# Kernel tuning notes

Hardware: AMD Instinct MI355X
Metric: run time of the kernel (lower is better)

## Reference

```python
import jax, jax.numpy as jnp
import numpy as np

EPS = 1e-5

def conv1x1(x, w, b):
    # x: [B,Cin,H,W], w: [Cout,Cin], b: [Cout]
    return jnp.einsum('oi,bihw->bohw', w, x) + b[None, :, None, None]

def self_attention(x, qw, qb, kw, kb, vw, vb, fw, fb):
    B, C, H, W = x.shape
    hid = qw.shape[0]
    q = conv1x1(x, qw, qb).reshape(B, hid, H * W).transpose(0, 2, 1)   # [B,HW,hid]
    k = conv1x1(x, kw, kb).reshape(B, hid, H * W)                      # [B,hid,HW]
    v = conv1x1(x, vw, vb).reshape(B, C, H * W)                        # [B,C,HW]
    attn = jax.nn.softmax(jnp.einsum('bnh,bhm->bnm', q, k), axis=-1)   # [B,HW,HW]
    z = jnp.einsum('bnm,bcm->bnc', attn, v)                            # [B,HW,C]
    # faithful to torch .view(B,C,H,W) on contiguous [B,HW,C]: raw reshape, no transpose
    z = z.reshape(B, C, H, W)
    return conv1x1(z * x, fw, fb) + x

def group_norm_per_channel(y, gw, gb):
    # GroupNorm(num_groups == num_channels): per-channel instance norm, biased var
    mean = y.mean(axis=(2, 3), keepdims=True)
    var = ((y - mean) ** 2).mean(axis=(2, 3), keepdims=True)
    yn = (y - mean) * jax.lax.rsqrt(var + EPS)
    return yn * gw[None, :, None, None] + gb[None, :, None, None]

def setup_inputs() -> dict:
    key = jax.random.key(0)
    ks = jax.random.split(key, 32)
    B, C, H, W = 4, 64, 64, 64
    hid, att = 64, 64
    d = {}
    d['x'] = jax.random.normal(ks[0], (B, C, H, W), jnp.float32)
    d['h'] = jax.random.normal(ks[1], (B, hid, H, W), jnp.float32)
    d['c'] = jax.random.normal(ks[2], (B, hid, H, W), jnp.float32)
    i = 3
    for pre, cin in (('ax', C), ('ah', hid)):
        for nm, cout in (('q', att), ('k', att), ('v', cin), ('f', cin)):
            d[f'{pre}_{nm}w'] = jax.random.normal(ks[i], (cout, cin), jnp.float32) * 0.05; i += 1
            d[f'{pre}_{nm}b'] = jax.random.normal(ks[i], (cout,), jnp.float32) * 0.05; i += 1
    d['conv_w'] = jax.random.normal(ks[i], (4 * hid, C + hid, 3, 3), jnp.float32) * 0.05; i += 1
    d['conv_b'] = jax.random.normal(ks[i], (4 * hid,), jnp.float32) * 0.05; i += 1
    d['gn_w'] = jnp.ones((4 * hid,), jnp.float32)
    d['gn_b'] = jnp.zeros((4 * hid,), jnp.float32)
    return d

def reference(x, h, c,
              ax_qw, ax_qb, ax_kw, ax_kb, ax_vw, ax_vb, ax_fw, ax_fb,
              ah_qw, ah_qb, ah_kw, ah_kb, ah_vw, ah_vb, ah_fw, ah_fb,
              conv_w, conv_b, gn_w, gn_b):
    hid = h.shape[1]
    xa = self_attention(x, ax_qw, ax_qb, ax_kw, ax_kb, ax_vw, ax_vb, ax_fw, ax_fb)
    ha = self_attention(h, ah_qw, ah_qb, ah_kw, ah_kb, ah_vw, ah_vb, ah_fw, ah_fb)
    combined = jnp.concatenate([xa, ha], axis=1)
    y = jax.lax.conv_general_dilated(
        combined, conv_w, window_strides=(1, 1), padding=[(1, 1), (1, 1)],
        dimension_numbers=('NCHW', 'OIHW', 'NCHW')) + conv_b[None, :, None, None]
    y = group_norm_per_channel(y, gn_w, gn_b)
    i, f, o, g = jnp.split(y, 4, axis=1)
    i = jax.nn.sigmoid(i); f = jax.nn.sigmoid(f); o = jax.nn.sigmoid(o); g = jnp.tanh(g)
    c_next = f * c + i * g
    h_next = o * jnp.tanh(c_next)
    return jnp.stack([h_next, c_next])  # [2,B,hid,H,W]
```

## Files before the change

kernel.cpp:

```cpp
#include <hip/hip_runtime.h>
#include <hip/hip_bf16.h>


typedef __hip_bfloat16 bf16;
typedef const __hip_bfloat16* bfp;
typedef short bf16x8 __attribute__((ext_vector_type(8)));
typedef short short4v __attribute__((ext_vector_type(4)));
typedef float f32x4 __attribute__((ext_vector_type(4)));
typedef float f32x16 __attribute__((ext_vector_type(16)));
typedef unsigned int u32x4 __attribute__((ext_vector_type(4)));

#define SM_SHIFT 12.0f
#define SM_A  184.66496523378733f
#define SM_B  14034.452417194552f

__device__ __forceinline__ float ldf(const void* p, long i, int f32) {
    return f32 ? ((const float*)p)[i]
               : __bfloat162float(((const bf16*)p)[i]);
}
__device__ __forceinline__ short f2bf(float f) {
    bf16 h = __float2bfloat16(f);
    return *reinterpret_cast<short*>(&h);
}
__device__ __forceinline__ float bfv(short s) {
    unsigned short u = (unsigned short)s;
    return __bfloat162float(*reinterpret_cast<const bf16*>(&u));
}

__device__ __forceinline__ int sniff_f32(const void* xr)
{
    int lane = threadIdx.x & 63;
    unsigned long long v = ((const unsigned long long*)xr)[lane];
    int ok = 0;
#pragma unroll
    for (int i = 0; i < 4; ++i) {
        int e = (int)((v >> (16 * i + 7)) & 0xFF);
        ok += (e >= 100 && e <= 141);
    }
    ok += __shfl_xor(ok, 1, 64);
    ok += __shfl_xor(ok, 2, 64);
    ok += __shfl_xor(ok, 4, 64);
    ok += __shfl_xor(ok, 8, 64);
    ok += __shfl_xor(ok, 16, 64);
    ok += __shfl_xor(ok, 32, 64);
    return ok < 200;
}

__global__ __launch_bounds__(256) void qkv_kernel(
    const void* __restrict__ Xx, const void* __restrict__ Xh,
    const void* __restrict__ qwx, const void* __restrict__ qbx,
    const void* __restrict__ kwx, const void* __restrict__ kbx,
    const void* __restrict__ vwx, const void* __restrict__ vbx,
    const void* __restrict__ qwh, const void* __restrict__ qbh,
    const void* __restrict__ kwh, const void* __restrict__ kbh,
    const void* __restrict__ vwh, const void* __restrict__ vbh,
    bf16* __restrict__ Qx, bf16* __restrict__ Kx, bf16* __restrict__ Vtx,
    bf16* __restrict__ Qh, bf16* __restrict__ Kh, bf16* __restrict__ Vth,
    const void* __restrict__ cw, bf16* __restrict__ Wt,
    float* __restrict__ gacc, int qkvN)
{
    __shared__ __align__(16) short xt[64][72];
    __shared__ __align__(16) short wq[64][72];
    __shared__ __align__(16) short wk[64][72];
    __shared__ __align__(16) short wv[64][72];
    int bx = blockIdx.x;
    int tid = threadIdx.x;
    int f32 = sniff_f32(Xx);
    if (bx >= qkvN) {
        if (bx == qkvN) {
            for (int j = 0; j < 8; ++j)
                gacc[tid * 8 + j] = 0.f;
        }
        short* tl = &xt[0][0];
        int t = bx - qkvN;
        long sbase = (long)t * 2304;
        if (!f32) {
            const short* cw16 = (const short*)cw;
            for (int j = tid; j < 288; j += 256) {
                bf16x8 v = *(const bf16x8*)(cw16 + sbase + j * 8);
#pragma unroll
                for (int e = 0; e < 8; ++e) {
                    int local = j * 8 + e;
                    int ocl = local / 1152, rem = local % 1152;
                    int ic = rem / 9, tap = rem % 9;
                    tl[ocl * 1152 + tap * 128 + ic] = v[e];
                }
            }
        } else {
            for (int j = tid; j < 2304; j += 256) {
                int ocl = j / 1152, rem = j % 1152;
                int ic = rem / 9, tap = rem % 9;
                tl[ocl * 1152 + tap * 128 + ic] =
                    f2bf(((const float*)cw)[sbase + j]);
            }
        }
        __syncthreads();
        for (int j = tid; j < 288; j += 256) {
            int d = j * 8;
            int ocl = d / 1152, rem = d % 1152;
            int tap = rem / 128, ic0 = rem % 128;
            bf16x8 v = *(const bf16x8*)(tl + ocl * 1152 + tap * 128 + ic0);
            *(bf16x8*)((short*)Wt + (long)tap * 32768
                       + (long)(t * 2 + ocl) * 128 + ic0) = v;
        }
        return;
    }
    int ab  = (bx >> 8) & 1;
    int idx = bx & 255;
    int b = idx >> 6;
    int n0 = (idx & 63) * 64;
    int wave = tid >> 6, lane = tid & 63;
    int q = lane >> 4, l15 = lane & 15;

    const void* X = ab ? Xh : Xx;
    const void* qw = ab ? qwh : qwx; const void* qb = ab ? qbh : qbx;
    const void* kw = ab ? kwh : kwx; const void* kb = ab ? kbh : kbx;
    const void* vw = ab ? vwh : vwx; const void* vb = ab ? vbh : vbx;
    short* Qg  = (short*)(ab ? Qh  : Qx)  + (long)b * 262144;
    short* Kg  = (short*)(ab ? Kh  : Kx)  + (long)b * 262144;
    short* Vtg = (short*)(ab ? Vth : Vtx) + (long)b * 262144;

    if (!f32) {
        const short* q16 = (const short*)qw;
        const short* k16 = (const short*)kw;
        const short* v16 = (const short*)vw;
        for (int rep = 0; rep < 2; ++rep) {
            int j8 = (rep * 256 + tid) * 8;
            *(bf16x8*)&wq[j8 >> 6][j8 & 63] = *(const bf16x8*)(q16 + j8);
            *(bf16x8*)&wk[j8 >> 6][j8 & 63] = *(const bf16x8*)(k16 + j8);
            *(bf16x8*)&wv[j8 >> 6][j8 & 63] = *(const bf16x8*)(v16 + j8);
        }
    } else {
        for (int rep = 0; rep < 16; ++rep) {
            int j = rep * 256 + tid;
            int i = j >> 6, cc = j & 63;
            wq[i][cc] = f2bf(((const float*)qw)[j]);
            wk[i][cc] = f2bf(((const float*)kw)[j]);
            wv[i][cc] = f2bf(((const float*)vw)[j]);
        }
    }
    long xbase = (long)b * 262144;
    if (!f32) {
        const short* X16 = (const short*)X;
        for (int rep = 0; rep < 2; ++rep) {
            int c = rep * 32 + (tid >> 3);
            int p8 = (tid & 7) * 8;
            bf16x8 v = *(const bf16x8*)(X16 + xbase + (long)c * 4096 + n0 + p8);
#pragma unroll
            for (int j = 0; j < 8; ++j) xt[p8 + j][c] = v[j];
        }
    } else {
        for (int rep = 0; rep < 16; ++rep) {
            int c = rep * 4 + (tid >> 6);
            int p = tid & 63;
            xt[p][c] = f2bf(ldf(X, xbase + (long)c * 4096 + n0 + p, f32));
        }
    }
    __syncthreads();

    bf16x8 a0 = *(const bf16x8*)&xt[wave * 16 + l15][q * 8];
    bf16x8 a1 = *(const bf16x8*)&xt[wave * 16 + l15][32 + q * 8];

    float qreg[4][4], kreg[4][4];
    for (int ct = 0; ct < 4; ++ct) {
        bf16x8 bq0 = *(const bf16x8*)&wq[ct * 16 + l15][q * 8];
        bf16x8 bq1 = *(const bf16x8*)&wq[ct * 16 + l15][32 + q * 8];
        f32x4 z = (f32x4){0.f, 0.f, 0.f, 0.f};
        z = __builtin_amdgcn_mfma_f32_16x16x32_bf16(a0, bq0, z, 0, 0, 0);
        z = __builtin_amdgcn_mfma_f32_16x16x32_bf16(a1, bq1, z, 0, 0, 0);
        float bias = ldf(qb, ct * 16 + l15, f32);
        for (int reg = 0; reg < 4; ++reg) qreg[ct][reg] = z[reg] + bias;
    }
    for (int ct = 0; ct < 4; ++ct) {
        bf16x8 bk0 = *(const bf16x8*)&wk[ct * 16 + l15][q * 8];
        bf16x8 bk1 = *(const bf16x8*)&wk[ct * 16 + l15][32 + q * 8];
        f32x4 z = (f32x4){0.f, 0.f, 0.f, 0.f};
        z = __builtin_amdgcn_mfma_f32_16x16x32_bf16(a0, bk0, z, 0, 0, 0);
        z = __builtin_amdgcn_mfma_f32_16x16x32_bf16(a1, bk1, z, 0, 0, 0);
        float bias = ldf(kb, ct * 16 + l15, f32);
        for (int reg = 0; reg < 4; ++reg) kreg[ct][reg] = z[reg] + bias;
    }
    __syncthreads();
#pragma unroll
    for (int ct = 0; ct < 4; ++ct)
#pragma unroll
        for (int reg = 0; reg < 4; ++reg) {
            wq[wave * 16 + q * 4 + reg][ct * 16 + l15] = f2bf(qreg[ct][reg]);
            wk[wave * 16 + q * 4 + reg][ct * 16 + l15] = f2bf(kreg[ct][reg]);
        }
    __syncthreads();
    {
        int r = tid >> 2;
        int c0 = (tid & 3) * 16;
        *(bf16x8*)(Qg + (long)(n0 + r) * 64 + c0)     = *(const bf16x8*)&wq[r][c0];
        *(bf16x8*)(Qg + (long)(n0 + r) * 64 + c0 + 8) = *(const bf16x8*)&wq[r][c0 + 8];
        *(bf16x8*)(Kg + (long)(n0 + r) * 64 + c0)     = *(const bf16x8*)&wk[r][c0];
        *(bf16x8*)(Kg + (long)(n0 + r) * 64 + c0 + 8) = *(const bf16x8*)&wk[r][c0 + 8];
    }
    bf16x8 av0 = *(const bf16x8*)&wv[wave * 16 + l15][q * 8];
    bf16x8 av1 = *(const bf16x8*)&wv[wave * 16 + l15][32 + q * 8];
    for (int ct = 0; ct < 4; ++ct) {
        bf16x8 bx0 = *(const bf16x8*)&xt[ct * 16 + l15][q * 8];
        bf16x8 bx1 = *(const bf16x8*)&xt[ct * 16 + l15][32 + q * 8];
        f32x4 z = (f32x4){0.f, 0.f, 0.f, 0.f};
        z = __builtin_amdgcn_mfma_f32_16x16x32_bf16(av0, bx0, z, 0, 0, 0);
        z = __builtin_amdgcn_mfma_f32_16x16x32_bf16(av1, bx1, z, 0, 0, 0);
        for (int reg = 0; reg < 4; ++reg) {
            int c_out = wave * 16 + q * 4 + reg;
            float bias = ldf(vb, c_out, f32);
            Vtg[(long)c_out * 4096 + n0 + ct * 16 + l15] = f2bf(z[reg] + bias);
        }
    }
}

__global__ __launch_bounds__(512, 4) void attn_kernel(
    bfp Qx, bfp Kx, bfp Vtx,
    const void* __restrict__ Xx, const void* __restrict__ fwx,
    const void* __restrict__ fbx, bf16* __restrict__ outx,
    bfp Qh, bfp Kh, bfp Vth,
    const void* __restrict__ Xh, const void* __restrict__ fwh,
    const void* __restrict__ fbh, bf16* __restrict__ outh)
{
    __shared__ __align__(16) short smem[32768];

    int tid = threadIdx.x;
    int wave = tid >> 6, lane = tid & 63;
    int l31 = lane & 31, hi = lane >> 5;
    int nh = wave >> 2, mq = wave & 3;
    int bid = blockIdx.x;
    int ab, b, hrow;
    if (gridDim.x == 512) {
        int abb = bid & 7;
        ab = abb >> 2; b = abb & 3;
        hrow = bid >> 3;
    } else {
        ab = 0; b = bid & 3;
        hrow = bid >> 2;
    }
    int f32 = sniff_f32(Xx);

    const short* Qb  = (const short*)(ab ? Qh  : Qx)  + (long)b * 262144;
    const short* Kb  = (const short*)(ab ? Kh  : Kx)  + (long)b * 262144;
    const short* Vtb = (const short*)(ab ? Vth : Vtx) + (long)b * 262144;
    const void* X  = ab ? Xh  : Xx;
    const void* fw = ab ? fwh : fwx;
    const void* fb = ab ? fbh : fbx;
    bf16* out = ab ? outh : outx;
    long xbase = (long)b * 262144;

    int cnq = nh * 32 + l31;
    long nq = (long)cnq * 64 + hrow;
    bf16x8 aq[4];
#pragma unroll
    for (int kc = 0; kc < 4; ++kc)
        aq[kc] = *(const bf16x8*)(Qb + nq * 64 + kc * 16 + hi * 8);

    f32x16 acc[2];
    acc[0] = (f32x16)(0.0f); acc[1] = (f32x16)(0.0f);
    f32x16 acc_l = (f32x16)(0.0f);
    const short ONE = 0x3F80;
    const bf16x8 ones = {ONE, ONE, ONE, ONE, ONE, ONE, ONE, ONE};

    int krow = mq * 32 + l31;
    int swk = ((krow >> 1) ^ (krow >> 4)) & 7;
    int cR0 = l31, cR1 = 32 + l31;
    int kv0 = (cR0 ^ (cR0 >> 3)) & 7;
    int kv1 = (cR1 ^ (cR1 >> 3)) & 7;

    int r0 = tid >> 3, r1 = r0 + 64;
    int g = tid & 7;
    int sr0 = (r0 & 51) | ((r0 & 4) << 1) | ((r0 & 8) >> 1);
    int sr1 = sr0 + 64;
    int gk0 = (g ^ (((sr0 >> 1) ^ (sr0 >> 4)) & 7)) << 3;
    int gk1 = (g ^ (((sr1 >> 1) ^ (sr1 >> 4)) & 7)) << 3;
    int cV = r0;
    int gv = (g ^ ((cV ^ (cV >> 3)) & 7)) << 3;

    bf16x8 pk0 = *(const bf16x8*)(Kb + (long)r0 * 64 + g * 8);
    bf16x8 pk1 = *(const bf16x8*)(Kb + (long)r1 * 64 + g * 8);
    bf16x8 pv0 = *(const bf16x8*)(Vtb + (long)cV * 4096 + g * 8);
    bf16x8 pv1 = *(const bf16x8*)(Vtb + (long)cV * 4096 + 64 + g * 8);

    for (int mt = 0; mt < 32; ++mt) {
        int buf = mt & 1;
        short* ksw = smem + buf * 8192;
        short* vsw = smem + 16384 + buf * 8192;
        *(bf16x8*)(ksw + sr0 * 64 + gk0)     = pk0;
        *(bf16x8*)(ksw + sr1 * 64 + gk1)     = pk1;
        *(bf16x8*)(vsw + cV * 128 + gv)      = pv0;
        *(bf16x8*)(vsw + cV * 128 + gv + 64) = pv1;
        __syncthreads();
        if (mt + 1 < 32) {
            long m = (long)(mt + 1) * 128;
            pk0 = *(const bf16x8*)(Kb + (m + r0) * 64 + g * 8);
            pk1 = *(const bf16x8*)(Kb + (m + r1) * 64 + g * 8);
            pv0 = *(const bf16x8*)(Vtb + (long)cV * 4096 + m + g * 8);
            pv1 = *(const bf16x8*)(Vtb + (long)cV * 4096 + m + 64 + g * 8);
        }
        const short* ksb  = smem + buf * 8192;
        const short* vtsb = smem + 16384 + buf * 8192;

        f32x16 s = (f32x16)(0.0f);
        const short* kbase = ksb + krow * 64;
#pragma unroll
        for (int kc = 0; kc < 4; ++kc) {
            bf16x8 ak = *(const bf16x8*)(kbase + (((kc * 2 + hi) ^ swk) << 3));
            s = __builtin_amdgcn_mfma_f32_32x32x16_bf16(ak, aq[kc], s, 0, 0, 0);
        }

        unsigned P32[8];
#pragma unroll
        for (int i = 0; i < 8; ++i) {
            unsigned b0 = (unsigned)fmaxf(fmaf(s[2 * i],     SM_A, SM_B), 0.f);
            unsigned b1 = (unsigned)fmaxf(fmaf(s[2 * i + 1], SM_A, SM_B), 0.f);
            P32[i] = b0 | (b1 << 16);
        }
        u32x4 B0v = (u32x4){P32[0], P32[1], P32[2], P32[3]};
        u32x4 B1v = (u32x4){P32[4], P32[5], P32[6], P32[7]};
        bf16x8 bp0 = __builtin_bit_cast(bf16x8, B0v);
        bf16x8 bp1 = __builtin_bit_cast(bf16x8, B1v);

        acc_l = __builtin_amdgcn_mfma_f32_32x32x16_bf16(ones, bp0, acc_l, 0, 0, 0);
        acc_l = __builtin_amdgcn_mfma_f32_32x32x16_bf16(ones, bp1, acc_l, 0, 0, 0);

#pragma unroll
        for (int mc = 0; mc < 2; ++mc) {
            bf16x8 bp = mc ? bp1 : bp0;
            int qch = mq * 4 + mc * 2 + hi;
            bf16x8 av0 = *(const bf16x8*)(
                vtsb + cR0 * 128 + ((qch ^ kv0) << 3));
            bf16x8 av1 = *(const bf16x8*)(
                vtsb + cR1 * 128 + ((qch ^ kv1) << 3));
            acc[0] = __builtin_amdgcn_mfma_f32_32x32x16_bf16(av0, bp, acc[0], 0, 0, 0);
            acc[1] = __builtin_amdgcn_mfma_f32_32x32x16_bf16(av1, bp, acc[1], 0, 0, 0);
        }
    }

    float l_acc = acc_l[0];

    float* fs = (float*)smem;
    float* fl = (float*)smem + 8192;
    short* fwt_s = smem + 16896;
    short* o_lds = smem + 21504;
    short* at_s  = smem;

    __syncthreads();
    if (hi == 0) fl[nh * 128 + mq * 32 + l31] = l_acc;
    if (mq == 1 || mq == 3) {
        int L = mq >> 1;
#pragma unroll
        for (int ch = 0; ch < 2; ++ch)
#pragma unroll
            for (int r = 0; r < 16; ++r) {
                int c = ch * 32 + (r & 3) + ((r >> 2) << 3) + (hi << 2);
                fs[L * 4096 + nh * 2048 + c * 32 + l31] = acc[ch][r];
            }
    }
    if (!f32) {
        int j8 = tid * 8;
        *(bf16x8*)(fwt_s + (j8 >> 6) * 72 + (j8 & 63)) =
            *(const bf16x8*)((const short*)fw + j8);
    } else {
#pragma unroll
        for (int jj = 0; jj < 8; ++jj) {
            int j = tid * 8 + jj;
            fwt_s[(j >> 6) * 72 + (j & 63)] = f2bf(((const float*)fw)[j]);
        }
    }
    __syncthreads();
    if (mq == 0 || mq == 2) {
        int L = mq >> 1;
#pragma unroll
        for (int ch = 0; ch < 2; ++ch)
#pragma unroll
            for (int r = 0; r < 16; ++r) {
                int c = ch * 32 + (r & 3) + ((r >> 2) << 3) + (hi << 2);
                acc[ch][r] += fs[L * 4096 + nh * 2048 + c * 32 + l31];
            }
    }
    __syncthreads();
    if (mq == 2) {
#pragma unroll
        for (int ch = 0; ch < 2; ++ch)
#pragma unroll
            for (int r = 0; r < 16; ++r) {
                int c = ch * 32 + (r & 3) + ((r >> 2) << 3) + (hi << 2);
                fs[nh * 2048 + c * 32 + l31] = acc[ch][r];
            }
    }
    __syncthreads();
    if (mq == 0) {
        float l_tot = fl[nh * 128 + l31]      + fl[nh * 128 + 32 + l31]
                    + fl[nh * 128 + 64 + l31] + fl[nh * 128 + 96 + l31];
        float iln = 1.f / l_tot;
        short* orow = o_lds + cnq * 68;
#pragma unroll
        for (int ch = 0; ch < 2; ++ch)
#pragma unroll
            for (int rq = 0; rq < 4; ++rq) {
                short4v o4;
#pragma unroll
                for (int j = 0; j < 4; ++j) {
                    int r = rq * 4 + j;
                    int c = ch * 32 + (r & 3) + ((r >> 2) << 3) + (hi << 2);
                    o4[j] = f2bf((acc[ch][r] +
                                  fs[nh * 2048 + c * 32 + l31]) * iln);
                }
                *(short4v*)(orow + ch * 32 + rq * 8 + hi * 4) = o4;
            }
    }
    __syncthreads();
    {
        int cn = tid >> 3;
        int w8 = (tid & 7) * 8;
        if (!f32) {
            bf16x8 xv = *(const bf16x8*)(
                (const short*)X + xbase + (long)cn * 4096 + hrow * 64 + w8);
#pragma unroll
            for (int j = 0; j < 8; ++j)
                at_s[(w8 + j) * 78 + cn] =
                    f2bf(bfv(o_lds[cn * 68 + w8 + j]) * bfv(xv[j]));
        } else {
#pragma unroll
            for (int j = 0; j < 8; ++j)
                at_s[(w8 + j) * 78 + cn] =
                    f2bf(bfv(o_lds[cn * 68 + w8 + j]) *
                         ((const float*)X)[xbase + (long)cn * 4096 + hrow * 64 + w8 + j]);
        }
    }
    __syncthreads();
    {
        int q = lane >> 4, l15 = lane & 15;
        int w4 = wave & 3;
        int ntb = (wave >> 2) * 2;
        bf16x8 a0 = *(const bf16x8*)(fwt_s + (w4 * 16 + l15) * 72 + q * 8);
        bf16x8 a1 = *(const bf16x8*)(fwt_s + (w4 * 16 + l15) * 72 + 32 + q * 8);
        short* outp = (short*)out;
        for (int nt = ntb; nt < ntb + 2; ++nt) {
            bf16x8 b0 = *(const bf16x8*)(at_s + (nt * 16 + l15) * 78 + q * 8);
            bf16x8 b1 = *(const bf16x8*)(at_s + (nt * 16 + l15) * 78 + 32 + q * 8);
            f32x4 z = (f32x4){0.f, 0.f, 0.f, 0.f};
            z = __builtin_amdgcn_mfma_f32_16x16x32_bf16(a0, b0, z, 0, 0, 0);
            z = __builtin_amdgcn_mfma_f32_16x16x32_bf16(a1, b1, z, 0, 0, 0);
            int w = nt * 16 + l15;
            short4v o4;
            for (int reg = 0; reg < 4; ++reg) {
                int o = w4 * 16 + q * 4 + reg;
                float v = z[reg] + ldf(fb, o, f32) +
                          ldf(X, xbase + (long)o * 4096 + hrow * 64 + w, f32);
                o4[reg] = f2bf(v);
            }
            *(short4v*)(outp + (((long)(b * 64 + hrow) * 64 + w) * 64
                                + w4 * 16 + q * 4)) = o4;
        }
    }
}

__global__ __launch_bounds__(512) void conv3x3_kernel(
    bfp xa, bfp ha, bfp Wt, const void* __restrict__ cb,
    bf16* __restrict__ y, float* __restrict__ gacc,
    const void* __restrict__ xraw)
{
    __shared__ __align__(16) short in_s[3][66][136];
    int f32 = sniff_f32(xraw);
    int bx = blockIdx.x;
    int b = bx >> 6;
    int h = bx & 63;
    int tid = threadIdx.x;
    int wave = tid >> 6, lane = tid & 63;
    int q = lane >> 4, l15 = lane & 15;

    const short* xab = (const short*)xa + (long)b * 262144;
    const short* hab = (const short*)ha + (long)b * 262144;
    const bf16x8 zv = {0, 0, 0, 0, 0, 0, 0, 0};
    for (int r = 0; r < 3; ++r) {
        int gy = h + r - 1;
        bool valid = (gy >= 0) && (gy < 64);
        int w = tid >> 3;
        int c8 = (tid & 7) * 8;
        bf16x8 vx = zv, vh = zv;
        if (valid) {
            vx = *(const bf16x8*)(xab + ((long)gy * 64 + w) * 64 + c8);
            vh = *(const bf16x8*)(hab + ((long)gy * 64 + w) * 64 + c8);
        }
        *(bf16x8*)&in_s[r][w + 1][c8]      = vx;
        *(bf16x8*)&in_s[r][w + 1][64 + c8] = vh;
    }
    if (tid < 96) {
        int r = tid / 32;
        int rest = tid % 32;
        int col = (rest & 1) ? 65 : 0;
        int c8 = (rest >> 1) * 8;
        *(bf16x8*)&in_s[r][col][c8] = zv;
    }
    __syncthreads();

    int oc0 = wave * 32;
    f32x4 acc[2][4];
    for (int mt = 0; mt < 2; ++mt)
        for (int nt = 0; nt < 4; ++nt)
            acc[mt][nt] = (f32x4){0.f, 0.f, 0.f, 0.f};

    const short* Wb = (const short*)Wt;
    for (int tap = 0; tap < 9; ++tap) {
        int dy = tap / 3, dx = tap - dy * 3;
        for (int kc = 0; kc < 4; ++kc) {
            bf16x8 afrag[2];
            for (int mt = 0; mt < 2; ++mt)
                afrag[mt] = *(const bf16x8*)(
                    Wb + ((long)tap * 256 + oc0 + mt * 16 + l15) * 128 + kc * 32 + q * 8);
            for (int nt = 0; nt < 4; ++nt) {
                bf16x8 bfrag = *(const bf16x8*)&in_s[dy][nt * 16 + l15 + dx][kc * 32 + q * 8];
                for (int mt = 0; mt < 2; ++mt)
                    acc[mt][nt] = __builtin_amdgcn_mfma_f32_16x16x32_bf16(
                        afrag[mt], bfrag, acc[mt][nt], 0, 0, 0);
            }
        }
    }

    long ybase = (long)b * 1048576 + (long)h * 64;
    for (int mt = 0; mt < 2; ++mt) {
        for (int reg = 0; reg < 4; ++reg) {
            int oc = oc0 + mt * 16 + q * 4 + reg;
            float bias = ldf(cb, oc, f32);
            float s = 0.f, s2 = 0.f;
            for (int nt = 0; nt < 4; ++nt) {
                float v = acc[mt][nt][reg] + bias;
                ((short*)y)[ybase + (long)oc * 4096 + nt * 16 + l15] = f2bf(v);
                s += v; s2 = fmaf(v, v, s2);
            }
            s  += __shfl_xor(s,  1, 64);  s2 += __shfl_xor(s2, 1, 64);
            s  += __shfl_xor(s,  2, 64);  s2 += __shfl_xor(s2, 2, 64);
            s  += __shfl_xor(s,  4, 64);  s2 += __shfl_xor(s2, 4, 64);
            s  += __shfl_xor(s,  8, 64);  s2 += __shfl_xor(s2, 8, 64);
            if (l15 == 0) {
                atomicAdd(&gacc[b * 256 + oc], s);
                atomicAdd(&gacc[1024 + b * 256 + oc], s2);
            }
        }
    }
}

__global__ __launch_bounds__(256) void gates_kernel(
    bfp y, const float* __restrict__ gacc,
    const void* __restrict__ gw, const void* __restrict__ gb,
    const void* __restrict__ c_in, void* __restrict__ out)
{
    int f32 = sniff_f32(c_in);
    int t = blockIdx.x * 256 + threadIdx.x;
    int b = t >> 15;
    int r = t & 32767;
    int ch = r >> 9;
    int p8 = (r & 511) * 8;
    long ybase = (long)b * 1048576;
    long idx8 = (long)b * 262144 + (long)ch * 4096 + p8;

    float mu[4], rstd[4], gwv[4], gbv[4];
    bf16x8 yv[4];
#pragma unroll
    for (int g = 0; g < 4; ++g) {
        int cc = g * 64 + ch;
        float m = gacc[b * 256 + cc] * (1.f / 4096.f);
        float var = gacc[1024 + b * 256 + cc] * (1.f / 4096.f) - m * m;
        mu[g] = m;
        rstd[g] = rsqrtf(fmaxf(var, 0.f) + 1e-5f);
        gwv[g] = ldf(gw, cc, f32);
        gbv[g] = ldf(gb, cc, f32);
        yv[g] = *(const bf16x8*)((const short*)y + ybase + (long)cc * 4096 + p8);
    }
    float cprev[8];
    if (!f32) {
        bf16x8 cv = *(const bf16x8*)((const short*)c_in + idx8);
#pragma unroll
        for (int j = 0; j < 8; ++j) cprev[j] = bfv(cv[j]);
    } else {
#pragma unroll
        for (int j = 0; j < 8; ++j) cprev[j] = ((const float*)c_in)[idx8 + j];
    }
    bf16x8 hn8, cn8;
    float hnf[8], cnf[8];
#pragma unroll
    for (int j = 0; j < 8; ++j) {
        float v0 = (bfv(yv[0][j]) - mu[0]) * rstd[0] * gwv[0] + gbv[0];
        float v1 = (bfv(yv[1][j]) - mu[1]) * rstd[1] * gwv[1] + gbv[1];
        float v2 = (bfv(yv[2][j]) - mu[2]) * rstd[2] * gwv[2] + gbv[2];
        float v3 = (bfv(yv[3][j]) - mu[3]) * rstd[3] * gwv[3] + gbv[3];
        float ig = 1.f / (1.f + __expf(-v0));
        float fg = 1.f / (1.f + __expf(-v1));
        float og = 1.f / (1.f + __expf(-v2));
        float gg = tanhf(v3);
        float cn = fg * cprev[j] + ig * gg;
        float hn = og * tanhf(cn);
        hn8[j] = f2bf(hn); cn8[j] = f2bf(cn);
        hnf[j] = hn; cnf[j] = cn;
    }
    if (f32) {
        float* o32 = (float*)out;
#pragma unroll
        for (int j = 0; j < 8; ++j) {
            o32[idx8 + j] = hnf[j];
            o32[1048576 + idx8 + j] = cnf[j];
        }
    } else {
        short* o16 = (short*)out;
        *(bf16x8*)(o16 + idx8) = hn8;
        *(bf16x8*)(o16 + 1048576 + idx8) = cn8;
    }
}

extern "C" void kernel_launch(void* const* d_in, const int* in_sizes, int n_in,
                              void* d_out, int out_size, void* d_ws, size_t ws_size,
                              hipStream_t stream)
{
    const void* x = d_in[0]; const void* h = d_in[1]; const void* c = d_in[2];
    const void* ax_qw = d_in[3],  *ax_qb = d_in[4];
    const void* ax_kw = d_in[5],  *ax_kb = d_in[6];
    const void* ax_vw = d_in[7],  *ax_vb = d_in[8];
    const void* ax_fw = d_in[9],  *ax_fb = d_in[10];
    const void* ah_qw = d_in[11], *ah_qb = d_in[12];
    const void* ah_kw = d_in[13], *ah_kb = d_in[14];
    const void* ah_vw = d_in[15], *ah_vb = d_in[16];
    const void* ah_fw = d_in[17], *ah_fb = d_in[18];
    const void* conv_w = d_in[19], *conv_b = d_in[20];
    const void* gn_w = d_in[21],  *gn_b = d_in[22];

    char* wsb = (char*)d_ws;
    auto S = [&](int i) { return wsb + ((unsigned long)i << 21); };
    bool fused = ws_size >= (18ul << 20) + 16384;

    bf16* ha = (bf16*)S(0);
    bf16* Wt = (bf16*)S(1);
    bf16 *Qx, *Kx, *Vtx, *Qh, *Kh, *Vth, *xa, *y;
    char* tail;
    if (fused) {
        Qx = (bf16*)S(2); Kx = (bf16*)S(3); Vtx = (bf16*)S(4);
        Qh = (bf16*)S(5); Kh = (bf16*)S(6); Vth = (bf16*)S(7);
        xa = (bf16*)S(8); y = Qx;
        tail = S(9);
    } else {
        Qx = (bf16*)S(2); Kx = (bf16*)S(3); Vtx = (bf16*)S(4);
        Qh = Qx; Kh = Kx; Vth = Vtx;
        xa = (bf16*)S(6); y = Qx;
        tail = S(7);
    }
    float* gacc = (float*)tail;

    if (fused) {
        qkv_kernel<<<512 + 128, 256, 0, stream>>>(
            x, h,
            ax_qw, ax_qb, ax_kw, ax_kb, ax_vw, ax_vb,
            ah_qw, ah_qb, ah_kw, ah_kb, ah_vw, ah_vb,
            Qx, Kx, Vtx, Qh, Kh, Vth, conv_w, Wt, gacc, 512);
        attn_kernel<<<512, 512, 0, stream>>>(
            Qx, Kx, Vtx, x, ax_fw, ax_fb, xa,
            Qh, Kh, Vth, h, ah_fw, ah_fb, ha);
    } else {
        qkv_kernel<<<256 + 128, 256, 0, stream>>>(
            x, x,
            ax_qw, ax_qb, ax_kw, ax_kb, ax_vw, ax_vb,
            ax_qw, ax_qb, ax_kw, ax_kb, ax_vw, ax_vb,
            Qx, Kx, Vtx, Qx, Kx, Vtx, conv_w, Wt, gacc, 256);
        attn_kernel<<<256, 512, 0, stream>>>(
            Qx, Kx, Vtx, x, ax_fw, ax_fb, xa,
            Qx, Kx, Vtx, x, ax_fw, ax_fb, xa);
        qkv_kernel<<<256, 256, 0, stream>>>(
            h, h,
            ah_qw, ah_qb, ah_kw, ah_kb, ah_vw, ah_vb,
            ah_qw, ah_qb, ah_kw, ah_kb, ah_vw, ah_vb,
            Qh, Kh, Vth, Qh, Kh, Vth, conv_w, Wt, gacc, 256);
        attn_kernel<<<256, 512, 0, stream>>>(
            Qh, Kh, Vth, h, ah_fw, ah_fb, ha,
            Qh, Kh, Vth, h, ah_fw, ah_fb, ha);
    }
    conv3x3_kernel<<<256, 512, 0, stream>>>(xa, ha, Wt, conv_b, y, gacc, x);
    gates_kernel<<<512, 256, 0, stream>>>(y, gacc, gn_w, gn_b, c, d_out);
}
```

Baseline: 203.0 us.

## Fuse GroupNorm+LSTM gates into conv3x3 via grid-wide barrier, keep y in LDS

The conv3x3 kernel now keeps its output tile in shared memory instead of writing y to global memory. After a grid-wide atomic-counter barrier across all 256 blocks, it reads the finished per-channel statistics and applies GroupNorm and the LSTM gate math directly. This removes the separate gates kernel launch and the global round-trip of y. The barrier relies on all 256 blocks being co-resident and adds spin-wait latency. The counter is reset inside qkv_kernel, at gacc[2048], which matches the tail+8192 offset.

New measurement: 258.9 us. 27.5% more time.

```diff
diff --git a/kernel.cpp b/kernel.cpp
--- a/kernel.cpp
+++ b/kernel.cpp
@@ -70,6 +70,7 @@
         if (bx == qkvN) {
             for (int j = 0; j < 8; ++j)
                 gacc[tid * 8 + j] = 0.f;
+            if (tid == 0) ((unsigned*)gacc)[2048] = 0u;
         }
         short* tl = &xt[0][0];
         int t = bx - qkvN;
@@ -458,10 +459,12 @@
 
 __global__ __launch_bounds__(512) void conv3x3_kernel(
     bfp xa, bfp ha, bfp Wt, const void* __restrict__ cb,
-    bf16* __restrict__ y, float* __restrict__ gacc,
+    float* __restrict__ gacc, unsigned* __restrict__ cnt,
+    const void* __restrict__ gw, const void* __restrict__ gb,
+    const void* __restrict__ c_in, void* __restrict__ out,
     const void* __restrict__ xraw)
 {
-    __shared__ __align__(16) short in_s[3][66][136];
+    __shared__ __align__(16) short cs[26928];
     int f32 = sniff_f32(xraw);
     int bx = blockIdx.x;
     int b = bx >> 6;
@@ -483,15 +486,15 @@
             vx = *(const bf16x8*)(xab + ((long)gy * 64 + w) * 64 + c8);
             vh = *(const bf16x8*)(hab + ((long)gy * 64 + w) * 64 + c8);
         }
-        *(bf16x8*)&in_s[r][w + 1][c8]      = vx;
-        *(bf16x8*)&in_s[r][w + 1][64 + c8] = vh;
+        *(bf16x8*)(cs + r * 8976 + (w + 1) * 136 + c8)      = vx;
+        *(bf16x8*)(cs + r * 8976 + (w + 1) * 136 + 64 + c8) = vh;
     }
     if (tid < 96) {
         int r = tid / 32;
         int rest = tid % 32;
         int col = (rest & 1) ? 65 : 0;
         int c8 = (rest >> 1) * 8;
-        *(bf16x8*)&in_s[r][col][c8] = zv;
+        *(bf16x8*)(cs + r * 8976 + col * 136 + c8) = zv;
     }
     __syncthreads();
 
@@ -510,7 +513,8 @@
                 afrag[mt] = *(const bf16x8*)(
                     Wb + ((long)tap * 256 + oc0 + mt * 16 + l15) * 128 + kc * 32 + q * 8);
             for (int nt = 0; nt < 4; ++nt) {
-                bf16x8 bfrag = *(const bf16x8*)&in_s[dy][nt * 16 + l15 + dx][kc * 32 + q * 8];
+                bf16x8 bfrag = *(const bf16x8*)(
+                    cs + dy * 8976 + (nt * 16 + l15 + dx) * 136 + kc * 32 + q * 8);
                 for (int mt = 0; mt < 2; ++mt)
                     acc[mt][nt] = __builtin_amdgcn_mfma_f32_16x16x32_bf16(
                         afrag[mt], bfrag, acc[mt][nt], 0, 0, 0);
@@ -518,7 +522,8 @@
         }
     }
 
-    long ybase = (long)b * 1048576 + (long)h * 64;
+    __syncthreads();
+    short* y_s = cs;
     for (int mt = 0; mt < 2; ++mt) {
         for (int reg = 0; reg < 4; ++reg) {
             int oc = oc0 + mt * 16 + q * 4 + reg;
@@ -526,7 +531,7 @@
             float s = 0.f, s2 = 0.f;
             for (int nt = 0; nt < 4; ++nt) {
                 float v = acc[mt][nt][reg] + bias;
-                ((short*)y)[ybase + (long)oc * 4096 + nt * 16 + l15] = f2bf(v);
+                y_s[oc * 66 + nt * 16 + l15] = f2bf(v);
                 s += v; s2 = fmaf(v, v, s2);
             }
             s  += __shfl_xor(s,  1, 64);  s2 += __shfl_xor(s2, 1, 64);
@@ -539,72 +544,69 @@
             }
         }
     }
-}
-
-__global__ __launch_bounds__(256) void gates_kernel(
-    bfp y, const float* __restrict__ gacc,
-    const void* __restrict__ gw, const void* __restrict__ gb,
-    const void* __restrict__ c_in, void* __restrict__ out)
-{
-    int f32 = sniff_f32(c_in);
-    int t = blockIdx.x * 256 + threadIdx.x;
-    int b = t >> 15;
-    int r = t & 32767;
-    int ch = r >> 9;
-    int p8 = (r & 511) * 8;
-    long ybase = (long)b * 1048576;
-    long idx8 = (long)b * 262144 + (long)ch * 4096 + p8;
-
-    float mu[4], rstd[4], gwv[4], gbv[4];
-    bf16x8 yv[4];
-#pragma unroll
-    for (int g = 0; g < 4; ++g) {
-        int cc = g * 64 + ch;
-        float m = gacc[b * 256 + cc] * (1.f / 4096.f);
-        float var = gacc[1024 + b * 256 + cc] * (1.f / 4096.f) - m * m;
-        mu[g] = m;
-        rstd[g] = rsqrtf(fmaxf(var, 0.f) + 1e-5f);
-        gwv[g] = ldf(gw, cc, f32);
-        gbv[g] = ldf(gb, cc, f32);
-        yv[g] = *(const bf16x8*)((const short*)y + ybase + (long)cc * 4096 + p8);
-    }
-    float cprev[8];
-    if (!f32) {
-        bf16x8 cv = *(const bf16x8*)((const short*)c_in + idx8);
-#pragma unroll
-        for (int j = 0; j < 8; ++j) cprev[j] = bfv(cv[j]);
-    } else {
-#pragma unroll
-        for (int j = 0; j < 8; ++j) cprev[j] = ((const float*)c_in)[idx8 + j];
-    }
-    bf16x8 hn8, cn8;
-    float hnf[8], cnf[8];
-#pragma unroll
-    for (int j = 0; j < 8; ++j) {
-        float v0 = (bfv(yv[0][j]) - mu[0]) * rstd[0] * gwv[0] + gbv[0];
-        float v1 = (bfv(yv[1][j]) - mu[1]) * rstd[1] * gwv[1] + gbv[1];
-        float v2 = (bfv(yv[2][j]) - mu[2]) * rstd[2] * gwv[2] + gbv[2];
-        float v3 = (bfv(yv[3][j]) - mu[3]) * rstd[3] * gwv[3] + gbv[3];
-        float ig = 1.f / (1.f + __expf(-v0));
-        float fg = 1.f / (1.f + __expf(-v1));
-        float og = 1.f / (1.f + __expf(-v2));
-        float gg = tanhf(v3);
-        float cn = fg * cprev[j] + ig * gg;
-        float hn = og * tanhf(cn);
-        hn8[j] = f2bf(hn); cn8[j] = f2bf(cn);
-        hnf[j] = hn; cnf[j] = cn;
-    }
-    if (f32) {
-        float* o32 = (float*)out;
+    __threadfence();
+    if (tid == 0) {
+        atomicAdd(cnt, 1u);
+        while (atomicAdd(cnt, 0u) < 256u) { __builtin_amdgcn_s_sleep(8); }
+    }
+    __syncthreads();
+    __threadfence();
+
+    {
+        int ch = tid >> 3;
+        int px8 = (tid & 7) * 8;
+        float mu[4], rstd[4], gwv[4], gbv[4];
+        bf16x8 yv[4];
+#pragma unroll
+        for (int g = 0; g < 4; ++g) {
+            int cc = g * 64 + ch;
+            float m = gacc[b * 256 + cc] * (1.f / 4096.f);
+            float var = gacc[1024 + b * 256 + cc] * (1.f / 4096.f) - m * m;
+            mu[g] = m;
+            rstd[g] = rsqrtf(fmaxf(var, 0.f) + 1e-5f);
+            gwv[g] = ldf(gw, cc, f32);
+            gbv[g] = ldf(gb, cc, f32);
+            yv[g] = *(const bf16x8*)(y_s + (g * 64 + ch) * 66 + px8);
+        }
+        long idx8 = (long)b * 262144 + (long)ch * 4096 + h * 64 + px8;
+        float cprev[8];
+        if (!f32) {
+            bf16x8 cv = *(const bf16x8*)((const short*)c_in + idx8);
+#pragma unroll
+            for (int j = 0; j < 8; ++j) cprev[j] = bfv(cv[j]);
+        } else {
+#pragma unroll
+            for (int j = 0; j < 8; ++j) cprev[j] = ((const float*)c_in)[idx8 + j];
+        }
+        bf16x8 hn8, cn8;
+        float hnf[8], cnf[8];
 #pragma unroll
         for (int j = 0; j < 8; ++j) {
-            o32[idx8 + j] = hnf[j];
-            o32[1048576 + idx8 + j] = cnf[j];
-        }
-    } else {
-        short* o16 = (short*)out;
-        *(bf16x8*)(o16 + idx8) = hn8;
-        *(bf16x8*)(o16 + 1048576 + idx8) = cn8;
+            float v0 = (bfv(yv[0][j]) - mu[0]) * rstd[0] * gwv[0] + gbv[0];
+            float v1 = (bfv(yv[1][j]) - mu[1]) * rstd[1] * gwv[1] + gbv[1];
+            float v2 = (bfv(yv[2][j]) - mu[2]) * rstd[2] * gwv[2] + gbv[2];
+            float v3 = (bfv(yv[3][j]) - mu[3]) * rstd[3] * gwv[3] + gbv[3];
+            float ig = 1.f / (1.f + __expf(-v0));
+            float fg = 1.f / (1.f + __expf(-v1));
+            float og = 1.f / (1.f + __expf(-v2));
+            float gg = tanhf(v3);
+            float cn = fg * cprev[j] + ig * gg;
+            float hn = og * tanhf(cn);
+            hn8[j] = f2bf(hn); cn8[j] = f2bf(cn);
+            hnf[j] = hn; cnf[j] = cn;
+        }
+        if (f32) {
+            float* o32 = (float*)out;
+#pragma unroll
+            for (int j = 0; j < 8; ++j) {
+                o32[idx8 + j] = hnf[j];
+                o32[1048576 + idx8 + j] = cnf[j];
+            }
+        } else {
+            short* o16 = (short*)out;
+            *(bf16x8*)(o16 + idx8) = hn8;
+            *(bf16x8*)(o16 + 1048576 + idx8) = cn8;
+        }
     }
 }
 
@@ -630,20 +632,21 @@
 
     bf16* ha = (bf16*)S(0);
     bf16* Wt = (bf16*)S(1);
-    bf16 *Qx, *Kx, *Vtx, *Qh, *Kh, *Vth, *xa, *y;
+    bf16 *Qx, *Kx, *Vtx, *Qh, *Kh, *Vth, *xa;
     char* tail;
     if (fused) {
         Qx = (bf16*)S(2); Kx = (bf16*)S(3); Vtx = (bf16*)S(4);
         Qh = (bf16*)S(5); Kh = (bf16*)S(6); Vth = (bf16*)S(7);
-        xa = (bf16*)S(8); y = Qx;
+        xa = (bf16*)S(8);
         tail = S(9);
     } else {
         Qx = (bf16*)S(2); Kx = (bf16*)S(3); Vtx = (bf16*)S(4);
         Qh = Qx; Kh = Kx; Vth = Vtx;
-        xa = (bf16*)S(6); y = Qx;
+        xa = (bf16*)S(6);
         tail = S(7);
     }
     float* gacc = (float*)tail;
+    unsigned* cnt = (unsigned*)(tail + 8192);
 
     if (fused) {
         qkv_kernel<<<512 + 128, 256, 0, stream>>>(
@@ -672,6 +675,6 @@
             Qh, Kh, Vth, h, ah_fw, ah_fb, ha,
             Qh, Kh, Vth, h, ah_fw, ah_fb, ha);
     }
-    conv3x3_kernel<<<256, 512, 0, stream>>>(xa, ha, Wt, conv_b, y, gacc, x);
-    gates_kernel<<<512, 256, 0, stream>>>(y, gacc, gn_w, gn_b, c, d_out);
-}
+    conv3x3_kernel<<<256, 512, 0, stream>>>(
+        xa, ha, Wt, conv_b, gacc, cnt, gn_w, gn_b, c, d_out, x);
+}
```
